# Kernel tuning notes

Measured on AMD Instinct MI355X. Metric: run time of the kernel, lower is better.

## Reference

```python
import jax, jax.numpy as jnp
import numpy as np

B, H, W, C = 16, 32, 32, 512
HEADS, DHEAD = 8, 64  # head * channel == C
GROUPS, EPS = 32, 1e-5


def setup_inputs() -> dict:
    key = jax.random.key(0)
    ks = jax.random.split(key, 6)
    return {
        "x": jax.random.normal(ks[0], (B, H, W, C), jnp.float32),
        "gn_gamma": jnp.ones((C,), jnp.float32),
        "gn_beta": jnp.zeros((C,), jnp.float32),
        "wq": jax.random.normal(ks[1], (C, HEADS * DHEAD), jnp.float32) * 0.02,
        "wk": jax.random.normal(ks[2], (C, HEADS * DHEAD), jnp.float32) * 0.02,
        "wv": jax.random.normal(ks[3], (C, HEADS * DHEAD), jnp.float32) * 0.02,
        "conv_w": jax.random.normal(ks[4], (3, 3, HEADS * DHEAD, C), jnp.float32) * 0.02,
        "conv_b": jnp.zeros((C,), jnp.float32),
    }


def _group_norm(x, gamma, beta):
    b, h, w, c = x.shape
    xg = x.reshape(b, h, w, GROUPS, c // GROUPS)
    mean = jnp.mean(xg, axis=(1, 2, 4), keepdims=True)
    var = jnp.var(xg, axis=(1, 2, 4), keepdims=True)
    xn = (xg - mean) * jax.lax.rsqrt(var + EPS)
    return xn.reshape(b, h, w, c) * gamma + beta


def reference(x, gn_gamma, gn_beta, wq, wk, wv, conv_w, conv_b):
    xn = _group_norm(x, gn_gamma, gn_beta)          # [B,H,W,C]
    t = xn.reshape(B, H * W, C)                      # tokens [B,S,C]
    q = (t @ wq).reshape(B, H * W, HEADS, DHEAD)
    k = (t @ wk).reshape(B, H * W, HEADS, DHEAD)
    v = (t @ wv).reshape(B, H * W, HEADS, DHEAD)
    scale = 1.0 / jnp.sqrt(jnp.asarray(DHEAD, q.dtype))
    scores = jnp.einsum("bqhd,bkhd->bhqk", q, k) * scale  # [B,HEADS,S,S]
    weights = jax.nn.softmax(scores, axis=-1)
    out = jnp.einsum("bhqk,bkhd->bqhd", weights, v)       # [B,S,HEADS,DHEAD]
    out = out.reshape(B, H, W, HEADS * DHEAD)
    y = jax.lax.conv_general_dilated(
        out, conv_w, window_strides=(1, 1), padding=((1, 1), (1, 1)),
        dimension_numbers=("NHWC", "HWIO", "NHWC")) + conv_b
    return y + x
```

## Files before the change

### kernel.cpp

```cpp
#include <hip/hip_runtime.h>
#include <hip/hip_bf16.h>

#define Bn 16
#define Cc 512
#define Ss 1024
#define HEADS 8
#define DHEAD 64
#define GROUPS 32
#define CPG 16
#define EPSv 1e-5f
#define Mtok (Bn*Ss)
#define QKVS 1536
#define QKS 1024
#define PROW 34
#define PIMG (PROW*PROW)

typedef __hip_bfloat16 bf16;
typedef __attribute__((ext_vector_type(8))) short short8;
typedef __attribute__((ext_vector_type(4))) float f32x4;

union U4 { uint4 u; bf16 h[8]; };
union B4 { ushort4 u; bf16 h[4]; };

__device__ __forceinline__ void stage16(const bf16* g, bf16* l) {
    __builtin_amdgcn_global_load_lds((const __attribute__((address_space(1))) void*)g,
                                     (__attribute__((address_space(3))) void*)l,
                                     16, 0, 0);
}

__device__ __forceinline__ unsigned int pkbf(float a, float b) {
    union { __hip_bfloat16 h; unsigned short u; } ua, ub;
    ua.h = __float2bfloat16(a); ub.h = __float2bfloat16(b);
    return ((unsigned int)ub.u << 16) | ua.u;
}

__device__ __forceinline__ void swz_decode(int F, int& r, int& c) {
    int line = F >> 3, pos = F & 7;
    int u = pos ^ (line & 7);
    r = (line << 1) | (u >> 2);
    c = u & 3;
}
__device__ __forceinline__ int swz_off(int r, int q) {
    return (r >> 1) * 64 + (((((r & 1) << 2) + q) ^ ((r >> 1) & 7)) << 3);
}

__global__ __launch_bounds__(256) void wtrans3(const float* __restrict__ wq,
                                               const float* __restrict__ wk,
                                               const float* __restrict__ wv,
                                               bf16* __restrict__ dst) {
    const float* src = (blockIdx.y == 0) ? wq : (blockIdx.y == 1) ? wk : wv;
    size_t off = (size_t)blockIdx.y * 262144;
    int t = blockIdx.x * 256 + threadIdx.x;
    int n = t & 511, k8 = (t >> 9) * 8;
    const float* s = src + (size_t)k8 * 512 + n;
    U4 o;
#pragma unroll
    for (int j = 0; j < 8; j++) o.h[j] = __float2bfloat16(s[(size_t)j * 512]);
    *(uint4*)(dst + off + (size_t)n * 512 + k8) = o.u;
}

__global__ __launch_bounds__(256) void wtrans(const float* __restrict__ src,
                                              bf16* __restrict__ dst) {
    size_t off = (size_t)blockIdx.y * 262144;
    int t = blockIdx.x * 256 + threadIdx.x;
    int n = t & 511, k8 = (t >> 9) * 8;
    const float* s = src + off + (size_t)k8 * 512 + n;
    U4 o;
#pragma unroll
    for (int j = 0; j < 8; j++) o.h[j] = __float2bfloat16(s[(size_t)j * 512]);
    *(uint4*)(dst + off + (size_t)n * 512 + k8) = o.u;
}

__global__ __launch_bounds__(256) void gn_stats(const float* __restrict__ x,
                                                float* __restrict__ stats) {
    int bg = blockIdx.x;
    int b = bg >> 5, g = bg & 31;
    int tid = threadIdx.x;
    const size_t base = (size_t)b * Ss * Cc + g * CPG;
    float sum = 0.f, sq = 0.f;
    for (int i = tid; i < 4096; i += 256) {
        int s = i >> 2, c4 = (i & 3) * 4;
        float4 t = *(const float4*)(x + base + (size_t)s * Cc + c4);
        sum += t.x + t.y + t.z + t.w;
        sq  += t.x * t.x + t.y * t.y + t.z * t.z + t.w * t.w;
    }
    __shared__ float s1[4], s2[4];
#pragma unroll
    for (int off = 32; off > 0; off >>= 1) {
        sum += __shfl_down(sum, off);
        sq  += __shfl_down(sq,  off);
    }
    if ((tid & 63) == 0) { s1[tid >> 6] = sum; s2[tid >> 6] = sq; }
    __syncthreads();
    if (tid == 0) {
        float S = s1[0] + s1[1] + s1[2] + s1[3];
        float Q = s2[0] + s2[1] + s2[2] + s2[3];
        float mean = S * (1.f / 16384.f);
        float var  = Q * (1.f / 16384.f) - mean * mean;
        stats[bg * 2 + 0] = mean;
        stats[bg * 2 + 1] = rsqrtf(var + EPSv);
    }
}

__global__ __launch_bounds__(256) void gn_apply(const float* __restrict__ x,
                                                const float* __restrict__ stats,
                                                const float* __restrict__ gamma,
                                                const float* __restrict__ beta,
                                                bf16* __restrict__ xn) {
    size_t i = (size_t)blockIdx.x * 256 + threadIdx.x;
    size_t e = i * 4;
    int c0 = (int)(e & (Cc - 1));
    int token = (int)(e >> 9);
    int b = token >> 10;
    int g = c0 >> 4;
    float mean = stats[(b * 32 + g) * 2 + 0];
    float rstd = stats[(b * 32 + g) * 2 + 1];
    float4 t  = *(const float4*)(x + e);
    float4 gm = *(const float4*)(gamma + c0);
    float4 bt = *(const float4*)(beta + c0);
    B4 o;
    o.h[0] = __float2bfloat16((t.x - mean) * rstd * gm.x + bt.x);
    o.h[1] = __float2bfloat16((t.y - mean) * rstd * gm.y + bt.y);
    o.h[2] = __float2bfloat16((t.z - mean) * rstd * gm.z + bt.z);
    o.h[3] = __float2bfloat16((t.w - mean) * rstd * gm.w + bt.w);
    *(ushort4*)(xn + e) = o.u;
}

__global__ __launch_bounds__(256) void zero_pad(bf16* __restrict__ Pad) {
    int idx = blockIdx.x * 256 + threadIdx.x;
    int b = idx / (132 * 64);
    int rem = idx - b * 132 * 64;
    int t = rem >> 6, seg = rem & 63;
    int r, c;
    if (t < 34)      { r = 0;  c = t; }
    else if (t < 68) { r = 33; c = t - 34; }
    else { int u = t - 68; r = 1 + (u >> 1); c = (u & 1) * 33; }
    uint4 z = {0u, 0u, 0u, 0u};
    *(uint4*)(Pad + ((size_t)b * PIMG + r * PROW + c) * Cc + seg * 8) = z;
}

__global__ __launch_bounds__(256) void gemm_qkv(const bf16* __restrict__ A,
                                                const bf16* __restrict__ Wt,
                                                bf16* __restrict__ C,
                                                bf16* __restrict__ vT) {
    __shared__ __align__(16) bf16 As[2][4096];
    __shared__ __align__(16) bf16 Bs[2][4096];
    int tid = threadIdx.x;
    int wave = tid >> 6, lane = tid & 63;
    int l15 = lane & 15, quad = lane >> 4;
    int wm = wave >> 1, wn = wave & 1;
    int m0 = blockIdx.y * 128, n0 = blockIdx.x * 128;

    int r0_, c0_, r1_, c1_;
    swz_decode(wave * 128 + lane,      r0_, c0_);
    swz_decode(wave * 128 + 64 + lane, r1_, c1_);
    const bf16* gaS0 = A  + (size_t)(m0 + r0_) * Cc + c0_ * 8;
    const bf16* gaS1 = A  + (size_t)(m0 + r1_) * Cc + c1_ * 8;
    const bf16* gbS0 = Wt + (size_t)(n0 + r0_) * Cc + c0_ * 8;
    const bf16* gbS1 = Wt + (size_t)(n0 + r1_) * Cc + c1_ * 8;

    int aoffg[4], boffg[4];
#pragma unroll
    for (int mt = 0; mt < 4; mt++) aoffg[mt] = swz_off(wm * 64 + mt * 16 + l15, quad);
#pragma unroll
    for (int nt = 0; nt < 4; nt++) boffg[nt] = swz_off(wn * 64 + nt * 16 + l15, quad);

    auto stageg = [&](int k0, int p) {
        stage16(gaS0 + k0, &As[p][wave * 1024]);
        stage16(gaS1 + k0, &As[p][wave * 1024 + 512]);
        stage16(gbS0 + k0, &Bs[p][wave * 1024]);
        stage16(gbS1 + k0, &Bs[p][wave * 1024 + 512]);
    };

    f32x4 acc[4][4] = {};
    stageg(0, 0);
    for (int it = 0; it < 16; ++it) {
        int p = it & 1;
        if (it + 1 < 16) {
            stageg((it + 1) * 32, p ^ 1);
            asm volatile("s_waitcnt vmcnt(4)" ::: "memory");
        } else {
            asm volatile("s_waitcnt vmcnt(0)" ::: "memory");
        }
        __builtin_amdgcn_s_barrier();
        __builtin_amdgcn_sched_barrier(0);

        short8 af[4], bfv[4];
        af[0] = *(const short8*)&As[p][aoffg[0]];
#pragma unroll
        for (int nt = 0; nt < 4; nt++) bfv[nt] = *(const short8*)&Bs[p][boffg[nt]];
#pragma unroll
        for (int mt = 1; mt < 4; mt++) af[mt] = *(const short8*)&As[p][aoffg[mt]];

        __builtin_amdgcn_s_setprio(1);
#pragma unroll
        for (int mt = 0; mt < 3; mt++)
#pragma unroll
            for (int nt = 0; nt < 4; nt++)
                acc[mt][nt] = __builtin_amdgcn_mfma_f32_16x16x32_bf16(af[mt], bfv[nt], acc[mt][nt], 0, 0, 0);
        __builtin_amdgcn_s_setprio(0);
        asm volatile("s_waitcnt lgkmcnt(0)" ::: "memory");
        __builtin_amdgcn_s_barrier();
        __builtin_amdgcn_s_setprio(1);
#pragma unroll
        for (int nt = 0; nt < 4; nt++)
            acc[3][nt] = __builtin_amdgcn_mfma_f32_16x16x32_bf16(af[3], bfv[nt], acc[3][nt], 0, 0, 0);
        __builtin_amdgcn_s_setprio(0);
    }

    if (n0 < 1024) {
#pragma unroll
        for (int mt = 0; mt < 4; mt++)
#pragma unroll
            for (int r = 0; r < 4; r++) {
                size_t row = (size_t)(m0 + wm * 64 + mt * 16 + quad * 4 + r) * QKS + n0 + wn * 64 + l15;
#pragma unroll
                for (int nt = 0; nt < 4; nt++)
                    C[row + nt * 16] = __float2bfloat16(acc[mt][nt][r]);
            }
    } else {
        int hh = ((n0 - 1024) >> 6) + wn;
        int bq = m0 >> 10;
        int tok0 = (m0 & 1023) + wm * 64;
#pragma unroll
        for (int nt = 0; nt < 4; nt++) {
            int d = nt * 16 + l15;
            bf16* drow = vT + (size_t)(hh * 64 + d) * 16384 + bq * 1024 + tok0;
#pragma unroll
            for (int mt = 0; mt < 4; mt++) {
                B4 o;
#pragma unroll
                for (int r = 0; r < 4; r++) o.h[r] = __float2bfloat16(acc[mt][nt][r]);
                *(ushort4*)(drow + mt * 16 + quad * 4) = o.u;
            }
        }
    }
}

__global__ __launch_bounds__(256) void attention_mfma(const bf16* __restrict__ QK,
                                                      const bf16* __restrict__ vT,
                                                      bf16* __restrict__ Pad) {
    int blk = blockIdx.x;
    int qt = blk & 7;
    int bh = blk >> 3;
    int h = bh & (HEADS - 1), b = bh >> 3;
    int tid = threadIdx.x;
    int wave = tid >> 6, lane = tid & 63;
    int l15 = lane & 15, quad = lane >> 4;

    __shared__ __align__(16) bf16 KT[2][4096];
    __shared__ __align__(16) bf16 VTs[2][4096];

    const size_t base = (size_t)b * Ss * QKS + h * DHEAD;
    const bf16* kbase = QK + base + 512;

    int q0 = qt * 128 + wave * 32;
    const bf16* qrow = QK + base + (size_t)(q0 + l15) * QKS + quad * 8;
    short8 qfA0 = *(const short8*)(qrow);
    short8 qfA1 = *(const short8*)(qrow + 32);
    short8 qfB0 = *(const short8*)(qrow + 16 * QKS);
    short8 qfB1 = *(const short8*)(qrow + 16 * QKS + 32);

    int r1 = tid >> 3,         f1 = (tid & 7) ^ (r1 & 7);
    int r2 = (tid + 256) >> 3, f2 = ((tid + 256) & 7) ^ (r2 & 7);
    const bf16* gk1 = kbase + (size_t)r1 * QKS + f1 * 8;
    const bf16* gk2 = kbase + (size_t)r2 * QKS + f2 * 8;
    const bf16* gv1 = vT + (size_t)(h * 64 + r1) * 16384 + b * 1024 + f1 * 8;
    const bf16* gv2 = vT + (size_t)(h * 64 + r2) * 16384 + b * 1024 + f2 * 8;

    f32x4 oacc0[4] = {{0.f,0.f,0.f,0.f},{0.f,0.f,0.f,0.f},{0.f,0.f,0.f,0.f},{0.f,0.f,0.f,0.f}};
    f32x4 oacc1[4] = {{0.f,0.f,0.f,0.f},{0.f,0.f,0.f,0.f},{0.f,0.f,0.f,0.f},{0.f,0.f,0.f,0.f}};
    float lsum0 = 0.f, lsum1 = 0.f;
    const f32x4 zero4 = {0.f, 0.f, 0.f, 0.f};
    int srcA = ((quad & 1) * 2) * 16 + l15;
    int srcB = srcA + 16;
    bool hiq = (quad >= 2);
    int sw = l15 & 7;

    auto stage = [&](int c0, int p) {
        stage16(gk1 + (size_t)c0 * QKS, &KT[p][wave * 512]);
        stage16(gk2 + (size_t)c0 * QKS, &KT[p][2048 + wave * 512]);
        stage16(gv1 + c0,               &VTs[p][wave * 512]);
        stage16(gv2 + c0,               &VTs[p][2048 + wave * 512]);
    };

    stage(0, 0);
    for (int it = 0; it < 16; ++it) {
        int p = it & 1;
        if (it + 1 < 16) {
            stage((it + 1) * 64, p ^ 1);
            asm volatile("s_waitcnt vmcnt(4)" ::: "memory");
        } else {
            asm volatile("s_waitcnt vmcnt(0)" ::: "memory");
        }
        __builtin_amdgcn_s_barrier();
        __builtin_amdgcn_sched_barrier(0);

        unsigned int pk0[4][2], pk1[4][2];
        __builtin_amdgcn_s_setprio(1);
#pragma unroll
        for (int kb = 0; kb < 4; kb++) {
            const bf16* kr = &KT[p][(kb * 16 + l15) * 64];
            short8 kf0 = *(const short8*)(kr + ((quad ^ sw) * 8));
            short8 kf1 = *(const short8*)(kr + (((4 + quad) ^ sw) * 8));
            f32x4 s0 = __builtin_amdgcn_mfma_f32_16x16x32_bf16(kf0, qfA0, zero4, 0, 0, 0);
            s0 = __builtin_amdgcn_mfma_f32_16x16x32_bf16(kf1, qfA1, s0, 0, 0, 0);
            f32x4 s1 = __builtin_amdgcn_mfma_f32_16x16x32_bf16(kf0, qfB0, zero4, 0, 0, 0);
            s1 = __builtin_amdgcn_mfma_f32_16x16x32_bf16(kf1, qfB1, s1, 0, 0, 0);
            float a0 = __expf(s0[0] * 0.125f);
            float a1 = __expf(s0[1] * 0.125f);
            float a2 = __expf(s0[2] * 0.125f);
            float a3 = __expf(s0[3] * 0.125f);
            lsum0 += (a0 + a1) + (a2 + a3);
            pk0[kb][0] = pkbf(a0, a1);
            pk0[kb][1] = pkbf(a2, a3);
            float b0 = __expf(s1[0] * 0.125f);
            float b1 = __expf(s1[1] * 0.125f);
            float b2 = __expf(s1[2] * 0.125f);
            float b3 = __expf(s1[3] * 0.125f);
            lsum1 += (b0 + b1) + (b2 + b3);
            pk1[kb][0] = pkbf(b0, b1);
            pk1[kb][1] = pkbf(b2, b3);
        }
        __builtin_amdgcn_s_setprio(0);

        union { short8 s8; unsigned int u[4]; } PT00, PT01, PT10, PT11;
        {
            unsigned int A0 = __shfl((int)pk0[0][0], srcA), A1 = __shfl((int)pk0[0][1], srcA);
            unsigned int A2 = __shfl((int)pk0[1][0], srcA), A3 = __shfl((int)pk0[1][1], srcA);
            unsigned int B0 = __shfl((int)pk0[0][0], srcB), B1 = __shfl((int)pk0[0][1], srcB);
            unsigned int B2 = __shfl((int)pk0[1][0], srcB), B3 = __shfl((int)pk0[1][1], srcB);
            PT00.u[0] = hiq ? A2 : A0;  PT00.u[1] = hiq ? A3 : A1;
            PT00.u[2] = hiq ? B2 : B0;  PT00.u[3] = hiq ? B3 : B1;
            unsigned int C0 = __shfl((int)pk0[2][0], srcA), C1 = __shfl((int)pk0[2][1], srcA);
            unsigned int C2 = __shfl((int)pk0[3][0], srcA), C3 = __shfl((int)pk0[3][1], srcA);
            unsigned int D0 = __shfl((int)pk0[2][0], srcB), D1 = __shfl((int)pk0[2][1], srcB);
            unsigned int D2 = __shfl((int)pk0[3][0], srcB), D3 = __shfl((int)pk0[3][1], srcB);
            PT01.u[0] = hiq ? C2 : C0;  PT01.u[1] = hiq ? C3 : C1;
            PT01.u[2] = hiq ? D2 : D0;  PT01.u[3] = hiq ? D3 : D1;
        }
        {
            unsigned int A0 = __shfl((int)pk1[0][0], srcA), A1 = __shfl((int)pk1[0][1], srcA);
            unsigned int A2 = __shfl((int)pk1[1][0], srcA), A3 = __shfl((int)pk1[1][1], srcA);
            unsigned int B0 = __shfl((int)pk1[0][0], srcB), B1 = __shfl((int)pk1[0][1], srcB);
            unsigned int B2 = __shfl((int)pk1[1][0], srcB), B3 = __shfl((int)pk1[1][1], srcB);
            PT10.u[0] = hiq ? A2 : A0;  PT10.u[1] = hiq ? A3 : A1;
            PT10.u[2] = hiq ? B2 : B0;  PT10.u[3] = hiq ? B3 : B1;
            unsigned int C0 = __shfl((int)pk1[2][0], srcA), C1 = __shfl((int)pk1[2][1], srcA);
            unsigned int C2 = __shfl((int)pk1[3][0], srcA), C3 = __shfl((int)pk1[3][1], srcA);
            unsigned int D0 = __shfl((int)pk1[2][0], srcB), D1 = __shfl((int)pk1[2][1], srcB);
            unsigned int D2 = __shfl((int)pk1[3][0], srcB), D3 = __shfl((int)pk1[3][1], srcB);
            PT11.u[0] = hiq ? C2 : C0;  PT11.u[1] = hiq ? C3 : C1;
            PT11.u[2] = hiq ? D2 : D0;  PT11.u[3] = hiq ? D3 : D1;
        }

        __builtin_amdgcn_s_setprio(1);
#pragma unroll
        for (int dt = 0; dt < 4; dt++) {
            const bf16* vr = &VTs[p][(dt * 16 + l15) * 64];
            short8 vf0 = *(const short8*)(vr + ((quad ^ sw) * 8));
            short8 vf1 = *(const short8*)(vr + (((4 + quad) ^ sw) * 8));
            oacc0[dt] = __builtin_amdgcn_mfma_f32_16x16x32_bf16(vf0, PT00.s8, oacc0[dt], 0, 0, 0);
            oacc0[dt] = __builtin_amdgcn_mfma_f32_16x16x32_bf16(vf1, PT01.s8, oacc0[dt], 0, 0, 0);
            oacc1[dt] = __builtin_amdgcn_mfma_f32_16x16x32_bf16(vf0, PT10.s8, oacc1[dt], 0, 0, 0);
            oacc1[dt] = __builtin_amdgcn_mfma_f32_16x16x32_bf16(vf1, PT11.s8, oacc1[dt], 0, 0, 0);
        }
        __builtin_amdgcn_s_setprio(0);

        __builtin_amdgcn_sched_barrier(0);
        __builtin_amdgcn_s_barrier();
        __builtin_amdgcn_sched_barrier(0);
    }

    lsum0 += __shfl_xor(lsum0, 16);
    lsum0 += __shfl_xor(lsum0, 32);
    lsum1 += __shfl_xor(lsum1, 16);
    lsum1 += __shfl_xor(lsum1, 32);
    float inv0 = 1.f / lsum0;
    float inv1 = 1.f / lsum1;

    {
        int s = q0 + l15;
        size_t rowoff = ((size_t)(b * PROW + (s >> 5) + 1) * PROW + (s & 31) + 1) * Cc + h * DHEAD;
#pragma unroll
        for (int dt = 0; dt < 4; dt++) {
            B4 o;
#pragma unroll
            for (int r = 0; r < 4; r++) o.h[r] = __float2bfloat16(oacc0[dt][r] * inv0);
            *(ushort4*)(Pad + rowoff + dt * 16 + quad * 4) = o.u;
        }
    }
    {
        int s = q0 + 16 + l15;
        size_t rowoff = ((size_t)(b * PROW + (s >> 5) + 1) * PROW + (s & 31) + 1) * Cc + h * DHEAD;
#pragma unroll
        for (int dt = 0; dt < 4; dt++) {
            B4 o;
#pragma unroll
            for (int r = 0; r < 4; r++) o.h[r] = __float2bfloat16(oacc1[dt][r] * inv1);
            *(ushort4*)(Pad + rowoff + dt * 16 + quad * 4) = o.u;
        }
    }
}

__global__ __launch_bounds__(256, 2) void conv_mfma(const bf16* __restrict__ Pad,
                                                    const bf16* __restrict__ Wct,
                                                    const float* __restrict__ bias,
                                                    const float* __restrict__ xres,
                                                    float* __restrict__ out) {
    __shared__ __align__(16) bf16 As[2][136 * 32];
    __shared__ __align__(16) bf16 Bs[2][3 * 4096];

    int tid = threadIdx.x;
    int wave = tid >> 6, lane = tid & 63;
    int l15 = lane & 15, quad = lane >> 4;
    int wm = wave >> 1, wn = wave & 1;
    int m0 = blockIdx.y * 128, n0 = blockIdx.x * 128;
    int b = m0 >> 10, oh0 = (m0 & 1023) >> 5;

    int rA1, cA1, rA2, cA2, rA3, cA3;
    swz_decode(tid,              rA1, cA1);
    swz_decode(tid + 256,        rA2, cA2);
    swz_decode((tid & 31) + 512, rA3, cA3);
    int rr1 = rA1 / 34, co1 = rA1 - rr1 * 34;
    int rr2 = rA2 / 34, co2 = rA2 - rr2 * 34;
    int rr3 = rA3 / 34, co3 = rA3 - rr3 * 34;
    const size_t dyStride = (size_t)PROW * Cc;
    const bf16* pA1 = Pad + ((size_t)b * PIMG + (size_t)(oh0 + rr1) * PROW + co1) * Cc + cA1 * 8;
    const bf16* pA2 = Pad + ((size_t)b * PIMG + (size_t)(oh0 + rr2) * PROW + co2) * Cc + cA2 * 8;
    const bf16* pA3 = Pad + ((size_t)b * PIMG + (size_t)(oh0 + rr3) * PROW + co3) * Cc + cA3 * 8;

    int rB1, cB1, rB2, cB2;
    swz_decode(wave * 128 + lane,      rB1, cB1);
    swz_decode(wave * 128 + 64 + lane, rB2, cB2);
    const bf16* gw1 = Wct + (size_t)(n0 + rB1) * Cc + cB1 * 8;
    const bf16* gw2 = Wct + (size_t)(n0 + rB2) * Cc + cB2 * 8;

    int aoff[3][4], boff[4];
#pragma unroll
    for (int mt = 0; mt < 4; mt++) {
        int rbase = (wm * 2 + (mt >> 1)) * 34 + (mt & 1) * 16 + l15;
#pragma unroll
        for (int dxi = 0; dxi < 3; dxi++) aoff[dxi][mt] = swz_off(rbase + dxi, quad);
    }
#pragma unroll
    for (int nt = 0; nt < 4; nt++) boff[nt] = swz_off(wn * 64 + nt * 16 + l15, quad);

    auto stage_it = [&](int it, int p) {
        int dyi = it >> 4;
        int k0 = (it & 15) << 5;
        size_t ag = (size_t)dyi * dyStride + k0;
        stage16(pA1 + ag, &As[p][wave * 512]);
        stage16(pA2 + ag, &As[p][2048 + wave * 512]);
        if (tid < 32) stage16(pA3 + ag, &As[p][4096]);
        size_t wg = (size_t)(dyi * 3) * (Cc * Cc) + k0;
#pragma unroll
        for (int t = 0; t < 3; t++) {
            size_t tg = wg + (size_t)t * (Cc * Cc);
            stage16(gw1 + tg, &Bs[p][t * 4096 + wave * 1024]);
            stage16(gw2 + tg, &Bs[p][t * 4096 + wave * 1024 + 512]);
        }
    };

    f32x4 acc[4][4] = {};
    stage_it(0, 0);
    for (int it = 0; it < 48; ++it) {
        int p = it & 1;
        if (it + 1 < 48) {
            stage_it(it + 1, p ^ 1);
            asm volatile("s_waitcnt vmcnt(8)" ::: "memory");
        } else {
            asm volatile("s_waitcnt vmcnt(0)" ::: "memory");
        }
        __builtin_amdgcn_s_barrier();
        __builtin_amdgcn_sched_barrier(0);

        short8 af[3][4], bfv[3][4];
#pragma unroll
        for (int dxi = 0; dxi < 3; dxi++) {
#pragma unroll
            for (int mt = 0; mt < 4; mt++)
                af[dxi][mt] = *(const short8*)&As[p][aoff[dxi][mt]];
#pragma unroll
            for (int nt = 0; nt < 4; nt++)
                bfv[dxi][nt] = *(const short8*)&Bs[p][dxi * 4096 + boff[nt]];
        }

        __builtin_amdgcn_s_setprio(1);
#pragma unroll
        for (int dxi = 0; dxi < 2; dxi++)
#pragma unroll
            for (int mt = 0; mt < 4; mt++)
#pragma unroll
                for (int nt = 0; nt < 4; nt++)
                    acc[mt][nt] = __builtin_amdgcn_mfma_f32_16x16x32_bf16(af[dxi][mt], bfv[dxi][nt], acc[mt][nt], 0, 0, 0);
        __builtin_amdgcn_s_setprio(0);

        asm volatile("s_waitcnt lgkmcnt(0)" ::: "memory");
        __builtin_amdgcn_s_barrier();

        __builtin_amdgcn_s_setprio(1);
#pragma unroll
        for (int mt = 0; mt < 4; mt++)
#pragma unroll
            for (int nt = 0; nt < 4; nt++)
                acc[mt][nt] = __builtin_amdgcn_mfma_f32_16x16x32_bf16(af[2][mt], bfv[2][nt], acc[mt][nt], 0, 0, 0);
        __builtin_amdgcn_s_setprio(0);
    }

#pragma unroll
    for (int mt = 0; mt < 4; mt++)
#pragma unroll
        for (int r = 0; r < 4; r++) {
            size_t row = (size_t)(m0 + wm * 64 + mt * 16 + quad * 4 + r) * Cc + n0 + wn * 64 + l15;
#pragma unroll
            for (int nt = 0; nt < 4; nt++) {
                int n = n0 + wn * 64 + nt * 16 + l15;
                out[row + nt * 16] = acc[mt][nt][r] + bias[n] + xres[row + nt * 16];
            }
        }
}

extern "C" void kernel_launch(void* const* d_in, const int* in_sizes, int n_in,
                              void* d_out, int out_size, void* d_ws, size_t ws_size,
                              hipStream_t stream) {
    const float* x     = (const float*)d_in[0];
    const float* gamma = (const float*)d_in[1];
    const float* beta  = (const float*)d_in[2];
    const float* wq    = (const float*)d_in[3];
    const float* wk    = (const float*)d_in[4];
    const float* wv    = (const float*)d_in[5];
    const float* convw = (const float*)d_in[6];
    const float* convb = (const float*)d_in[7];
    float* out = (float*)d_out;

    char* ws = (char*)d_ws;
    bf16*  pad   = (bf16*)ws;
    float* stats = (float*)ws;
    bf16*  xn    = (bf16*)(ws + 4096);
    bf16*  wt    = (bf16*)(ws + 4096 + ((size_t)16 << 20));
    bf16*  qk    = (bf16*)(ws + ((size_t)19 << 20));
    bf16*  vt    = (bf16*)(ws + ((size_t)51 << 20));
    bf16*  wct   = (bf16*)(ws + ((size_t)67 << 20));

    wtrans3<<<dim3(128, 3), 256, 0, stream>>>(wq, wk, wv, wt);
    wtrans<<<dim3(128, 9), 256, 0, stream>>>(convw, wct);

    gn_stats<<<dim3(Bn * GROUPS), 256, 0, stream>>>(x, stats);
    gn_apply<<<dim3(Mtok * Cc / (4 * 256)), 256, 0, stream>>>(x, stats, gamma, beta, xn);

    gemm_qkv<<<dim3(QKVS / 128, Mtok / 128), 256, 0, stream>>>(xn, wt, qk, vt);

    zero_pad<<<dim3(528), 256, 0, stream>>>(pad);
    attention_mfma<<<dim3(Bn * HEADS * (Ss / 128)), 256, 0, stream>>>(qk, vt, pad);

    conv_mfma<<<dim3(Cc / 128, Mtok / 128), 256, 0, stream>>>(pad, wct, convb, x, out);
}
```

Before: 311.5 us.

## Enlarge conv implicit-GEMM tile to 256 rows and restructure the fragment loads

The conv kernel's M tile grows from 128 to 256 output pixels, i.e. 8 image rows per block, so each block covers 272 padded rows in shared memory and each wave holds 8x4 accumulators. Each weight tile is now reused across twice as many output rows, which halves weight traffic per output. The inner loop loads fragments per dx step instead of all at once, and the setprio hints are dropped. Launch bounds drop to one block per CU, which raises register and LDS use per block and halves the grid to 256 blocks, risking lower occupancy and less latency hiding.

After: 346.9 us. 11.4% more time.

```diff
diff --git a/kernel.cpp b/kernel.cpp
--- a/kernel.cpp
+++ b/kernel.cpp
@@ -403,32 +403,31 @@
     }
 }
 
-__global__ __launch_bounds__(256, 2) void conv_mfma(const bf16* __restrict__ Pad,
+__global__ __launch_bounds__(256, 1) void conv_mfma(const bf16* __restrict__ Pad,
                                                     const bf16* __restrict__ Wct,
                                                     const float* __restrict__ bias,
                                                     const float* __restrict__ xres,
                                                     float* __restrict__ out) {
-    __shared__ __align__(16) bf16 As[2][136 * 32];
+    __shared__ __align__(16) bf16 As[2][272 * 32];
     __shared__ __align__(16) bf16 Bs[2][3 * 4096];
 
     int tid = threadIdx.x;
     int wave = tid >> 6, lane = tid & 63;
     int l15 = lane & 15, quad = lane >> 4;
     int wm = wave >> 1, wn = wave & 1;
-    int m0 = blockIdx.y * 128, n0 = blockIdx.x * 128;
+    int m0 = blockIdx.y * 256, n0 = blockIdx.x * 128;
     int b = m0 >> 10, oh0 = (m0 & 1023) >> 5;
 
-    int rA1, cA1, rA2, cA2, rA3, cA3;
-    swz_decode(tid,              rA1, cA1);
-    swz_decode(tid + 256,        rA2, cA2);
-    swz_decode((tid & 31) + 512, rA3, cA3);
-    int rr1 = rA1 / 34, co1 = rA1 - rr1 * 34;
-    int rr2 = rA2 / 34, co2 = rA2 - rr2 * 34;
-    int rr3 = rA3 / 34, co3 = rA3 - rr3 * 34;
     const size_t dyStride = (size_t)PROW * Cc;
-    const bf16* pA1 = Pad + ((size_t)b * PIMG + (size_t)(oh0 + rr1) * PROW + co1) * Cc + cA1 * 8;
-    const bf16* pA2 = Pad + ((size_t)b * PIMG + (size_t)(oh0 + rr2) * PROW + co2) * Cc + cA2 * 8;
-    const bf16* pA3 = Pad + ((size_t)b * PIMG + (size_t)(oh0 + rr3) * PROW + co3) * Cc + cA3 * 8;
+    const bf16* pA[5];
+#pragma unroll
+    for (int s = 0; s < 5; s++) {
+        int F = (s < 4) ? (tid + s * 256) : (1024 + (tid & 63));
+        int rA, cA;
+        swz_decode(F, rA, cA);
+        int rr = rA / 34, co = rA - rr * 34;
+        pA[s] = Pad + ((size_t)b * PIMG + (size_t)(oh0 + rr) * PROW + co) * Cc + cA * 8;
+    }
 
     int rB1, cB1, rB2, cB2;
     swz_decode(wave * 128 + lane,      rB1, cB1);
@@ -436,10 +435,10 @@
     const bf16* gw1 = Wct + (size_t)(n0 + rB1) * Cc + cB1 * 8;
     const bf16* gw2 = Wct + (size_t)(n0 + rB2) * Cc + cB2 * 8;
 
-    int aoff[3][4], boff[4];
-#pragma unroll
-    for (int mt = 0; mt < 4; mt++) {
-        int rbase = (wm * 2 + (mt >> 1)) * 34 + (mt & 1) * 16 + l15;
+    int aoff[3][8], boff[4];
+#pragma unroll
+    for (int mt = 0; mt < 8; mt++) {
+        int rbase = (wm * 4 + (mt >> 1)) * 34 + (mt & 1) * 16 + l15;
 #pragma unroll
         for (int dxi = 0; dxi < 3; dxi++) aoff[dxi][mt] = swz_off(rbase + dxi, quad);
     }
@@ -450,9 +449,10 @@
         int dyi = it >> 4;
         int k0 = (it & 15) << 5;
         size_t ag = (size_t)dyi * dyStride + k0;
-        stage16(pA1 + ag, &As[p][wave * 512]);
-        stage16(pA2 + ag, &As[p][2048 + wave * 512]);
-        if (tid < 32) stage16(pA3 + ag, &As[p][4096]);
+#pragma unroll
+        for (int s = 0; s < 4; s++)
+            stage16(pA[s] + ag, &As[p][(wave * 64 + s * 256) * 8]);
+        stage16(pA[4] + ag, &As[p][(1024 + (tid & 63)) * 8]);
         size_t wg = (size_t)(dyi * 3) * (Cc * Cc) + k0;
 #pragma unroll
         for (int t = 0; t < 3; t++) {
@@ -462,57 +462,52 @@
         }
     };
 
-    f32x4 acc[4][4] = {};
+    f32x4 acc[8][4] = {};
     stage_it(0, 0);
     for (int it = 0; it < 48; ++it) {
         int p = it & 1;
         if (it + 1 < 48) {
             stage_it(it + 1, p ^ 1);
-            asm volatile("s_waitcnt vmcnt(8)" ::: "memory");
+            asm volatile("s_waitcnt vmcnt(11)" ::: "memory");
         } else {
             asm volatile("s_waitcnt vmcnt(0)" ::: "memory");
         }
         __builtin_amdgcn_s_barrier();
         __builtin_amdgcn_sched_barrier(0);
 
-        short8 af[3][4], bfv[3][4];
-#pragma unroll
-        for (int dxi = 0; dxi < 3; dxi++) {
-#pragma unroll
-            for (int mt = 0; mt < 4; mt++)
-                af[dxi][mt] = *(const short8*)&As[p][aoff[dxi][mt]];
+        short8 af[8], bfv[4];
+#pragma unroll
+        for (int dxi = 0; dxi < 2; dxi++) {
+#pragma unroll
+            for (int mt = 0; mt < 8; mt++) af[mt] = *(const short8*)&As[p][aoff[dxi][mt]];
+#pragma unroll
+            for (int nt = 0; nt < 4; nt++) bfv[nt] = *(const short8*)&Bs[p][dxi * 4096 + boff[nt]];
+#pragma unroll
+            for (int mt = 0; mt < 8; mt++)
+#pragma unroll
+                for (int nt = 0; nt < 4; nt++)
+                    acc[mt][nt] = __builtin_amdgcn_mfma_f32_16x16x32_bf16(af[mt], bfv[nt], acc[mt][nt], 0, 0, 0);
+        }
+        short8 af2[8], bfv2[4];
+#pragma unroll
+        for (int mt = 0; mt < 8; mt++) af2[mt] = *(const short8*)&As[p][aoff[2][mt]];
+#pragma unroll
+        for (int nt = 0; nt < 4; nt++) bfv2[nt] = *(const short8*)&Bs[p][2 * 4096 + boff[nt]];
+        asm volatile("s_waitcnt lgkmcnt(0)" ::: "memory");
+        __builtin_amdgcn_sched_barrier(0);
+        __builtin_amdgcn_s_barrier();
+#pragma unroll
+        for (int mt = 0; mt < 8; mt++)
 #pragma unroll
             for (int nt = 0; nt < 4; nt++)
-                bfv[dxi][nt] = *(const short8*)&Bs[p][dxi * 4096 + boff[nt]];
-        }
-
-        __builtin_amdgcn_s_setprio(1);
-#pragma unroll
-        for (int dxi = 0; dxi < 2; dxi++)
-#pragma unroll
-            for (int mt = 0; mt < 4; mt++)
-#pragma unroll
-                for (int nt = 0; nt < 4; nt++)
-                    acc[mt][nt] = __builtin_amdgcn_mfma_f32_16x16x32_bf16(af[dxi][mt], bfv[dxi][nt], acc[mt][nt], 0, 0, 0);
-        __builtin_amdgcn_s_setprio(0);
-
-        asm volatile("s_waitcnt lgkmcnt(0)" ::: "memory");
-        __builtin_amdgcn_s_barrier();
-
-        __builtin_amdgcn_s_setprio(1);
-#pragma unroll
-        for (int mt = 0; mt < 4; mt++)
-#pragma unroll
-            for (int nt = 0; nt < 4; nt++)
-                acc[mt][nt] = __builtin_amdgcn_mfma_f32_16x16x32_bf16(af[2][mt], bfv[2][nt], acc[mt][nt], 0, 0, 0);
-        __builtin_amdgcn_s_setprio(0);
-    }
-
-#pragma unroll
-    for (int mt = 0; mt < 4; mt++)
+                acc[mt][nt] = __builtin_amdgcn_mfma_f32_16x16x32_bf16(af2[mt], bfv2[nt], acc[mt][nt], 0, 0, 0);
+    }
+
+#pragma unroll
+    for (int mt = 0; mt < 8; mt++)
 #pragma unroll
         for (int r = 0; r < 4; r++) {
-            size_t row = (size_t)(m0 + wm * 64 + mt * 16 + quad * 4 + r) * Cc + n0 + wn * 64 + l15;
+            size_t row = (size_t)(m0 + wm * 128 + mt * 16 + quad * 4 + r) * Cc + n0 + wn * 64 + l15;
 #pragma unroll
             for (int nt = 0; nt < 4; nt++) {
                 int n = n0 + wn * 64 + nt * 16 + l15;
@@ -554,5 +549,5 @@
     zero_pad<<<dim3(528), 256, 0, stream>>>(pad);
     attention_mfma<<<dim3(Bn * HEADS * (Ss / 128)), 256, 0, stream>>>(qk, vt, pad);
 
-    conv_mfma<<<dim3(Cc / 128, Mtok / 128), 256, 0, stream>>>(pad, wct, convb, x, out);
-}
+    conv_mfma<<<dim3(Cc / 128, Mtok / 256), 256, 0, stream>>>(pad, wct, convb, x, out);
+}
```

## Load conv weight fragments directly from global into registers, bypassing LDS

Applied to the files above, without the earlier changes.

The conv kernel no longer stages weight tiles through shared memory. Each lane now loads its B fragments straight from global memory into double-buffered register arrays, prefetched one iteration ahead, and the main loop is unrolled by two so the two buffers alternate. This removes the LDS writes and reads for B and roughly halves shared memory use, which could allow more blocks per CU. In exchange it raises register pressure (24 extra short8 values), makes global loads less coalesced (each lane reads 16 bytes at a 1 KB row stride), and changes the vmcnt wait count, which must match the number of loads in flight.

After: 385.8 us. +23.8%, slower.

```diff
diff --git a/kernel.cpp b/kernel.cpp
--- a/kernel.cpp
+++ b/kernel.cpp
@@ -409,7 +409,6 @@
                                                     const float* __restrict__ xres,
                                                     float* __restrict__ out) {
     __shared__ __align__(16) bf16 As[2][136 * 32];
-    __shared__ __align__(16) bf16 Bs[2][3 * 4096];
 
     int tid = threadIdx.x;
     int wave = tid >> 6, lane = tid & 63;
@@ -430,61 +429,61 @@
     const bf16* pA2 = Pad + ((size_t)b * PIMG + (size_t)(oh0 + rr2) * PROW + co2) * Cc + cA2 * 8;
     const bf16* pA3 = Pad + ((size_t)b * PIMG + (size_t)(oh0 + rr3) * PROW + co3) * Cc + cA3 * 8;
 
-    int rB1, cB1, rB2, cB2;
-    swz_decode(wave * 128 + lane,      rB1, cB1);
-    swz_decode(wave * 128 + 64 + lane, rB2, cB2);
-    const bf16* gw1 = Wct + (size_t)(n0 + rB1) * Cc + cB1 * 8;
-    const bf16* gw2 = Wct + (size_t)(n0 + rB2) * Cc + cB2 * 8;
-
-    int aoff[3][4], boff[4];
+    int aoff[3][4];
 #pragma unroll
     for (int mt = 0; mt < 4; mt++) {
         int rbase = (wm * 2 + (mt >> 1)) * 34 + (mt & 1) * 16 + l15;
 #pragma unroll
         for (int dxi = 0; dxi < 3; dxi++) aoff[dxi][mt] = swz_off(rbase + dxi, quad);
     }
-#pragma unroll
-    for (int nt = 0; nt < 4; nt++) boff[nt] = swz_off(wn * 64 + nt * 16 + l15, quad);
-
-    auto stage_it = [&](int it, int p) {
+
+    const bf16* bp[4];
+#pragma unroll
+    for (int nt = 0; nt < 4; nt++)
+        bp[nt] = Wct + (size_t)(n0 + wn * 64 + nt * 16 + l15) * Cc + quad * 8;
+
+    auto stageA = [&](int it, int p) {
         int dyi = it >> 4;
         int k0 = (it & 15) << 5;
         size_t ag = (size_t)dyi * dyStride + k0;
         stage16(pA1 + ag, &As[p][wave * 512]);
         stage16(pA2 + ag, &As[p][2048 + wave * 512]);
         if (tid < 32) stage16(pA3 + ag, &As[p][4096]);
-        size_t wg = (size_t)(dyi * 3) * (Cc * Cc) + k0;
-#pragma unroll
-        for (int t = 0; t < 3; t++) {
-            size_t tg = wg + (size_t)t * (Cc * Cc);
-            stage16(gw1 + tg, &Bs[p][t * 4096 + wave * 1024]);
-            stage16(gw2 + tg, &Bs[p][t * 4096 + wave * 1024 + 512]);
-        }
     };
+    auto loadB = [&](int it, short8 (&bn)[12]) {
+        int dyi = it >> 4;
+        int k0 = (it & 15) << 5;
+        size_t tb = (size_t)(dyi * 3) * (Cc * Cc) + k0;
+#pragma unroll
+        for (int dxi = 0; dxi < 3; dxi++)
+#pragma unroll
+            for (int nt = 0; nt < 4; nt++)
+                bn[dxi * 4 + nt] = *(const short8*)(bp[nt] + tb + (size_t)dxi * (Cc * Cc));
+    };
 
     f32x4 acc[4][4] = {};
-    stage_it(0, 0);
-    for (int it = 0; it < 48; ++it) {
+    short8 bR0[12], bR1[12];
+    stageA(0, 0);
+    loadB(0, bR0);
+
+    auto body = [&](int it, short8 (&bc)[12], short8 (&bn)[12]) {
         int p = it & 1;
         if (it + 1 < 48) {
-            stage_it(it + 1, p ^ 1);
-            asm volatile("s_waitcnt vmcnt(8)" ::: "memory");
+            stageA(it + 1, p ^ 1);
+            loadB(it + 1, bn);
+            asm volatile("s_waitcnt vmcnt(26)" ::: "memory");
         } else {
             asm volatile("s_waitcnt vmcnt(0)" ::: "memory");
         }
         __builtin_amdgcn_s_barrier();
         __builtin_amdgcn_sched_barrier(0);
 
-        short8 af[3][4], bfv[3][4];
-#pragma unroll
-        for (int dxi = 0; dxi < 3; dxi++) {
+        short8 af[3][4];
+#pragma unroll
+        for (int dxi = 0; dxi < 3; dxi++)
 #pragma unroll
             for (int mt = 0; mt < 4; mt++)
                 af[dxi][mt] = *(const short8*)&As[p][aoff[dxi][mt]];
-#pragma unroll
-            for (int nt = 0; nt < 4; nt++)
-                bfv[dxi][nt] = *(const short8*)&Bs[p][dxi * 4096 + boff[nt]];
-        }
 
         __builtin_amdgcn_s_setprio(1);
 #pragma unroll
@@ -493,7 +492,7 @@
             for (int mt = 0; mt < 4; mt++)
 #pragma unroll
                 for (int nt = 0; nt < 4; nt++)
-                    acc[mt][nt] = __builtin_amdgcn_mfma_f32_16x16x32_bf16(af[dxi][mt], bfv[dxi][nt], acc[mt][nt], 0, 0, 0);
+                    acc[mt][nt] = __builtin_amdgcn_mfma_f32_16x16x32_bf16(af[dxi][mt], bc[dxi * 4 + nt], acc[mt][nt], 0, 0, 0);
         __builtin_amdgcn_s_setprio(0);
 
         asm volatile("s_waitcnt lgkmcnt(0)" ::: "memory");
@@ -504,8 +503,13 @@
         for (int mt = 0; mt < 4; mt++)
 #pragma unroll
             for (int nt = 0; nt < 4; nt++)
-                acc[mt][nt] = __builtin_amdgcn_mfma_f32_16x16x32_bf16(af[2][mt], bfv[2][nt], acc[mt][nt], 0, 0, 0);
+                acc[mt][nt] = __builtin_amdgcn_mfma_f32_16x16x32_bf16(af[2][mt], bc[8 + nt], acc[mt][nt], 0, 0, 0);
         __builtin_amdgcn_s_setprio(0);
+    };
+
+    for (int it2 = 0; it2 < 48; it2 += 2) {
+        body(it2,     bR0, bR1);
+        body(it2 + 1, bR1, bR0);
     }
 
 #pragma unroll
```
